# Kernel tuning notes

Hardware: AMD Instinct MI355X
Metric: run time of the kernel (lower is better)

Reference implementation:

```python
import jax, jax.numpy as jnp
import numpy as np

N = 200_000        # primal nodes (mesh faces)
E = 600_000        # directed primal edges (= dual nodes)
F = 128            # feature dim
NUM_KEEP = 300_000 # num_primal_edges_to_keep
ITERS = 40         # label-propagation iterations (>= ~2*log2(N), safely converged)


def setup_inputs() -> dict:
    key = jax.random.key(0)
    k1, k2, k3, k4 = jax.random.split(key, 4)
    primal_x = jax.random.normal(k1, (N, F), dtype=jnp.float32)
    dual_x = jax.random.normal(k2, (E, F), dtype=jnp.float32)
    att = jax.random.uniform(k3, (E,), dtype=jnp.float32)  # attention coeffs in (0,1)
    primal_edge_index = jax.random.randint(k4, (2, E), 0, N, dtype=jnp.int32)
    return {"primal_x": primal_x, "dual_x": dual_x, "att": att,
            "primal_edge_index": primal_edge_index}


def _pool(primal_x, dual_x, att, primal_edge_index):
    src, dst = primal_edge_index[0], primal_edge_index[1]
    num_pool = E - NUM_KEEP

    # --- Top-K edge selection by decreasing attention coefficient ---
    order = jnp.argsort(-att)
    pool_mask = jnp.zeros((E,), jnp.bool_).at[order[:num_pool]].set(True)

    # --- Union-find / connected components of pooled edges via
    #     min-label propagation with pointer jumping (vectorized union-find) ---
    u = src
    v = jnp.where(pool_mask, dst, src)  # masked edges become self-edges (no-ops)

    def body(_, l):
        l = l.at[u].min(l[v]).at[v].min(l[u])  # edge relaxations (scatter-min)
        l = l[l]                                # pointer jumping
        l = l[l]
        return l

    labels = jax.lax.fori_loop(0, ITERS, body, jnp.arange(N, dtype=jnp.int32))

    # --- Compact component labels into contiguous new-primal-node ids ---
    _, cluster = jnp.unique(labels, size=N, fill_value=N, return_inverse=True)
    cluster = cluster.astype(jnp.int32)

    # --- Aggregate primal node features per cluster ('mean') ---
    counts = jax.ops.segment_sum(jnp.ones((N,), primal_x.dtype), cluster,
                                 num_segments=N)
    new_primal_x = jax.ops.segment_sum(primal_x, cluster, num_segments=N)
    new_primal_x = new_primal_x / jnp.maximum(counts, 1.0)[:, None]

    # --- Rebuild primal edges; edges internal to a cluster are pooled away ---
    cu, cv = cluster[src], cluster[dst]
    valid = cu != cv
    new_primal_edge_index = jnp.stack([jnp.where(valid, cu, -1),
                                       jnp.where(valid, cv, -1)])

    # --- Dual nodes: one per (unordered) surviving new primal edge
    #     ('single' dual nodes); merge & mean-aggregate dual features of old
    #     dual nodes mapping to the same new dual node ---
    a = jnp.minimum(cu, cv)
    b = jnp.maximum(cu, cv)
    pairs = jnp.stack([jnp.where(valid, a, N), jnp.where(valid, b, N)], axis=1)
    _, dual_cluster = jnp.unique(pairs, axis=0, size=E, fill_value=N,
                                 return_inverse=True)
    dual_cluster = dual_cluster.reshape(E).astype(jnp.int32)
    vm = valid.astype(dual_x.dtype)
    dcounts = jax.ops.segment_sum(vm, dual_cluster, num_segments=E)
    new_dual_x = jax.ops.segment_sum(dual_x * vm[:, None], dual_cluster,
                                     num_segments=E)
    new_dual_x = new_dual_x / jnp.maximum(dcounts, 1.0)[:, None]

    return new_primal_x, new_dual_x, new_primal_edge_index, cluster


def reference(primal_x, dual_x, att, primal_edge_index):
    return _pool(primal_x, dual_x, att, primal_edge_index)
```

## Files before the change

### kernel.cpp

```cpp
#include <hip/hip_runtime.h>
#include <stdint.h>


#define N_NODES 200000
#define N_EDGES 600000
#define FDIM 128
#define NUM_POOL 300000u

#define SC_NEEDEQ 3
#define SC_TIECNT 4
#define SC_C 5
#define SC_W 6
#define SC_U 7
#define SC_VCNT 8
#define SC_WL0 16
#define TIECAP 4096
#define WLCAP 300800
#define HB 256
#define NSB 98
#define NSHAD 4
#define NSHAD2 16
#define CMAX 16384
#define SROWS 64
#define SGB 782
#define CS2B 128

__device__ __forceinline__ uint32_t f2ou(float f){
  uint32_t b = __float_as_uint(f);
  return (b & 0x80000000u) ? ~b : (b | 0x80000000u);
}

static __device__ __forceinline__ void sel_level(const uint32_t* hist, uint32_t& target,
                                                 uint32_t& pfx, uint32_t* sm, uint32_t* res){
  int t = threadIdx.x;
  uint32_t cnt = hist[t];
  sm[t] = cnt; __syncthreads();
  for(int off = 1; off < 256; off <<= 1){
    uint32_t y = (t + off < 256) ? sm[t + off] : 0u;
    __syncthreads(); sm[t] += y; __syncthreads();
  }
  uint32_t suffix = sm[t];
  uint32_t above  = suffix - cnt;
  if(above < target && target <= suffix){ res[0] = (uint32_t)t; res[1] = target - above; }
  __syncthreads();
  pfx = (pfx << 8) | res[0];
  target = res[1];
  __syncthreads();
}

static __device__ __forceinline__ uint32_t blk_excl(uint32_t v, uint32_t* sm, uint32_t& total){
  int t = threadIdx.x;
  sm[t] = v; __syncthreads();
  for(int off = 1; off < 256; off <<= 1){
    uint32_t y = (t >= off) ? sm[t - off] : 0u;
    __syncthreads(); sm[t] += y; __syncthreads();
  }
  total = sm[255];
  uint32_t incl = sm[t];
  __syncthreads();
  return incl - v;
}

__global__ __launch_bounds__(256) void k_zero(uint4* w4, uint32_t n4){
  uint32_t gid = blockIdx.x*256 + threadIdx.x;
  uint4 z = make_uint4(0u,0u,0u,0u);
  for(uint32_t j = gid; j < n4; j += gridDim.x*256) w4[j] = z;
}

template<int LEVEL>
__global__ __launch_bounds__(256) void k_hist8(const float* att, uint32_t* hists, int* L){
  __shared__ uint32_t h[256];
  __shared__ uint32_t sm[256];
  __shared__ uint32_t res[2];
  h[threadIdx.x] = 0;
  if(LEVEL == 1){
    for(int i = blockIdx.x*256 + threadIdx.x; i < N_NODES; i += HB*256) L[i] = i;
  }
  __syncthreads();
  uint32_t pfx = 0, target = NUM_POOL;
  #pragma unroll
  for(int l = 0; l < LEVEL-1; ++l) sel_level(hists + 256*l, target, pfx, sm, res);
  constexpr int SH1 = (LEVEL > 1) ? 8*(5-LEVEL) : 0;
  constexpr int SH2 = 8*(4-LEVEL);
  for(int e = blockIdx.x*256 + threadIdx.x; e < N_EDGES; e += HB*256){
    uint32_t u = f2ou(att[e]);
    bool ok = (LEVEL == 1) || ((u >> SH1) == pfx);
    if(ok) atomicAdd(&h[(u >> SH2) & 0xFFu], 1u);
  }
  __syncthreads();
  uint32_t c = h[threadIdx.x];
  if(c) atomicAdd(&hists[256*(LEVEL-1) + threadIdx.x], c);
}

__global__ __launch_bounds__(256) void k_seed(const float* att, const int* src, const int* dst,
                       const uint32_t* hists, uint32_t* sc, uint32_t* tieIdx, int* L, uint2* wl,
                       uint32_t* counts, uint32_t* counts2){
  __shared__ uint32_t sm[256];
  __shared__ uint32_t res[2];
  __shared__ uint32_t basesh;
  {
    uint32_t gid = blockIdx.x*256 + threadIdx.x;
    uint32_t gs = gridDim.x*256;
    const uint32_t TOTZ = N_NODES + CMAX*NSHAD2;
    for(uint32_t j = gid; j < TOTZ; j += gs){
      if(j < N_NODES) counts[j] = 0u; else counts2[j - N_NODES] = 0u;
    }
  }
  uint32_t pfx = 0, target = NUM_POOL;
  #pragma unroll
  for(int l = 0; l < 3; ++l) sel_level(hists + 256*l, target, pfx, sm, res);
  if(blockIdx.x == 0 && threadIdx.x == 0) sc[SC_NEEDEQ] = target;
  uint32_t T = pfx;
  int e = blockIdx.x*256 + threadIdx.x;
  bool app = false; int u = 0, v = 0;
  if(e < N_EDGES){
    uint32_t ub = f2ou(att[e]) >> 8;
    if(ub > T){
      u = src[e]; v = dst[e];
      if(u != v){
        int m = u < v ? u : v, hi = u ^ v ^ m;
        atomicMin(&L[hi], m);
        app = true;
      }
    } else if(ub == T){
      uint32_t p = atomicAdd(&sc[SC_TIECNT], 1u);
      if(p < TIECAP) tieIdx[p] = (uint32_t)e;
    }
  }
  uint32_t tot;
  uint32_t off = blk_excl(app ? 1u : 0u, sm, tot);
  if(threadIdx.x == 0 && tot) basesh = atomicAdd(&sc[SC_WL0], tot);
  __syncthreads();
  if(app) wl[basesh + off] = make_uint2((uint32_t)(u < v ? u : v), (uint32_t)(u > v ? u : v));
}

__global__ __launch_bounds__(256) void k_relax(const uint2* wl_in, uint2* wl_out, int* L,
                       uint32_t* sc, int inSlot, int outSlot,
                       const uint32_t* tieIdx, const float* att,
                       const int* src, const int* dst, int doTies){
  __shared__ uint32_t sm[256];
  __shared__ uint32_t basesh;
  uint32_t n = sc[inSlot];
  for(uint32_t base = blockIdx.x*256u; base < n; base += gridDim.x*256u){
    uint32_t idx = base + threadIdx.x;
    bool active = idx < n;
    int lu = 0, lv = 0;
    if(active){
      uint2 ed = wl_in[idx];
      lu = L[ed.x]; lu = L[lu]; lu = L[lu]; lu = L[lu];
      lv = L[ed.y]; lv = L[lv]; lv = L[lv]; lv = L[lv];
      active = (lu != lv);
      if(active){
        int m = lu < lv ? lu : lv, hi = lu ^ lv ^ m;
        atomicMin(&L[hi], m);
      }
    }
    uint32_t tot;
    uint32_t off = blk_excl(active ? 1u : 0u, sm, tot);
    if(threadIdx.x == 0 && tot) basesh = atomicAdd(&sc[outSlot], tot);
    __syncthreads();
    if(active) wl_out[basesh + off] = make_uint2((uint32_t)(lu < lv ? lu : lv),
                                                 (uint32_t)(lu > lv ? lu : lv));
    __syncthreads();
  }
  if(doTies && blockIdx.x == 0){
    uint32_t m = sc[SC_TIECNT]; if(m > TIECAP) m = TIECAP;
    uint32_t need = sc[SC_NEEDEQ];
    for(uint32_t i0 = 0; i0 < m; i0 += 256){
      uint32_t i = i0 + threadIdx.x;
      bool app = false; int u = 0, v = 0;
      if(i < m){
        uint32_t mine = tieIdx[i];
        uint32_t ki = f2ou(att[mine]);
        uint32_t r = 0;
        for(uint32_t j = 0; j < m; j++){
          uint32_t oj = tieIdx[j];
          uint32_t kj = f2ou(att[oj]);
          r += (kj > ki || (kj == ki && oj < mine)) ? 1u : 0u;
        }
        if(r < need){
          u = src[mine]; v = dst[mine];
          if(u != v){ int mm = u < v ? u : v, hi = u ^ v ^ mm; atomicMin(&L[hi], mm); app = true; }
        }
      }
      uint32_t tot;
      uint32_t off = blk_excl(app ? 1u : 0u, sm, tot);
      if(threadIdx.x == 0 && tot) basesh = atomicAdd(&sc[outSlot], tot);
      __syncthreads();
      if(app) wl_out[basesh + off] = make_uint2((uint32_t)(u < v ? u : v),
                                                (uint32_t)(u > v ? u : v));
      __syncthreads();
    }
  }
  if(n != 0){
    int i = blockIdx.x*256 + threadIdx.x;
    if(i < N_NODES){
      int v = L[i]; v = L[v]; v = L[v]; v = L[v];
      if(v < i) atomicMin(&L[i], v);
    }
  }
}
__global__ __launch_bounds__(256) void k_flatten_reduce(int* L, uint32_t* bsums){
  uint32_t base = blockIdx.x*2048u + threadIdx.x*8u;
  uint32_t s = 0;
  #pragma unroll
  for(int k = 0; k < 8; k++){
    uint32_t i = base + k;
    if(i < N_NODES){
      int p = L[i]; int q = L[p];
      while(q != p){ p = q; q = L[p]; }
      L[i] = p;
      s += (p == (int)i) ? 1u : 0u;
    }
  }
  __shared__ uint32_t sm[256];
  sm[threadIdx.x] = s; __syncthreads();
  for(int off = 128; off > 0; off >>= 1){
    if((int)threadIdx.x < off) sm[threadIdx.x] += sm[threadIdx.x + off];
    __syncthreads();
  }
  if(threadIdx.x == 0) bsums[blockIdx.x] = sm[0];
}

template<int MODE>
__device__ __forceinline__ uint32_t scan_n(const uint32_t* sc){
  if(MODE == 1) return sc[SC_W];
  if(MODE == 3) return sc[SC_C]*NSHAD2;
  return N_NODES;
}
template<int MODE>
__global__ __launch_bounds__(256) void k_scan_reduce(const uint32_t* in, uint32_t* bsums,
                       const uint32_t* sc, float* dsum, uint32_t* dcnt){
  uint32_t n = scan_n<MODE>(sc);
  if(MODE == 1){
    uint32_t vc = sc[SC_VCNT];
    size_t gid = (size_t)blockIdx.x*256 + threadIdx.x, gs = (size_t)gridDim.x*256;
    float4* d4 = (float4*)dsum;
    float4 z = make_float4(0.f,0.f,0.f,0.f);
    for(size_t j = gid; j < (size_t)vc*(FDIM/4); j += gs) d4[j] = z;
    for(size_t j = gid; j < vc; j += gs) dcnt[j] = 0u;
  }
  uint32_t base = blockIdx.x*2048u + threadIdx.x*8u;
  uint32_t s = 0;
  #pragma unroll
  for(int k = 0; k < 8; k++){
    uint32_t idx = base + k;
    if(idx < n){ uint32_t v = in[idx]; if(MODE == 1) v = __popc(v); s += v; }
  }
  __shared__ uint32_t sm[256];
  sm[threadIdx.x] = s; __syncthreads();
  for(int off = 128; off > 0; off >>= 1){
    if((int)threadIdx.x < off) sm[threadIdx.x] += sm[threadIdx.x + off];
    __syncthreads();
  }
  if(threadIdx.x == 0) bsums[blockIdx.x] = sm[0];
}
template<int MODE>
__global__ __launch_bounds__(256) void k_scan_apply(const uint32_t* in, const int* L,
                       const uint32_t* bsums, int nb, uint32_t* out, uint32_t* sc){
  __shared__ uint32_t bs[4096];
  __shared__ uint32_t sm[256];
  int t = threadIdx.x;
  uint32_t n = scan_n<MODE>(sc);
  uint32_t loc[16]; uint32_t ls = 0;
  #pragma unroll
  for(int k = 0; k < 16; k++){ int idx = t*16 + k; uint32_t v = (idx < nb) ? bsums[idx] : 0u; loc[k] = v; ls += v; }
  sm[t] = ls; __syncthreads();
  for(int off = 1; off < 256; off <<= 1){
    uint32_t y = (t >= off) ? sm[t - off] : 0u;
    __syncthreads(); sm[t] += y; __syncthreads();
  }
  uint32_t total = sm[255];
  uint32_t run = sm[t] - ls;
  #pragma unroll
  for(int k = 0; k < 16; k++){ bs[t*16 + k] = run; run += loc[k]; }
  __syncthreads();
  uint32_t blockbase = bs[blockIdx.x];
  __syncthreads();
  uint32_t base = blockIdx.x*2048u + t*8u;
  uint32_t xs[8]; uint32_t ts2 = 0;
  #pragma unroll
  for(int k = 0; k < 8; k++){
    uint32_t idx = base + k; uint32_t v = 0;
    if(idx < n){
      if(MODE == 2) v = (L[idx] == (int)idx) ? 1u : 0u;
      else { v = in[idx]; if(MODE == 1) v = __popc(v); }
    }
    xs[k] = v; ts2 += v;
  }
  sm[t] = ts2; __syncthreads();
  for(int off = 1; off < 256; off <<= 1){
    uint32_t y = (t >= off) ? sm[t - off] : 0u;
    __syncthreads(); sm[t] += y; __syncthreads();
  }
  uint32_t run2 = blockbase + sm[t] - ts2;
  #pragma unroll
  for(int k = 0; k < 8; k++){ uint32_t idx = base + k; if(idx < n) out[idx] = run2; run2 += xs[k]; }
  if(blockIdx.x == 0 && t == 0){
    if(MODE == 2){ sc[SC_C] = total; uint64_t cc = (uint64_t)total*(uint64_t)total; sc[SC_W] = (uint32_t)((cc + 31ull) >> 5); }
    if(MODE == 1){ sc[SC_U] = total; }
  }
}

__global__ __launch_bounds__(256) void k_cluster_counts(const int* L, const uint32_t* rank_,
                       int* cluster_i, float* outC, uint32_t* counts, uint32_t* counts2,
                       float* psumS, uint32_t* bitmap, const uint32_t* sc){
  uint32_t C = sc[SC_C], W = sc[SC_W];
  uint32_t gid = blockIdx.x*256 + threadIdx.x, gs = gridDim.x*256;
  float4* p4 = (float4*)psumS;
  float4 z = make_float4(0.f,0.f,0.f,0.f);
  for(size_t j = gid; j < (size_t)NSHAD*C*(FDIM/4); j += gs) p4[j] = z;
  for(uint32_t j = gid; j < W; j += gs) bitmap[j] = 0u;
  int i = (int)gid;
  int lane = threadIdx.x & 63;
  int sh = (int)((gid >> 6) & (NSHAD2-1));
  int c = -1;
  if(i < N_NODES){
    c = (int)rank_[L[i]];
    cluster_i[i] = c;
    outC[i] = (float)c;
  }
  unsigned long long remaining = __ballot(i < N_NODES);
  while(remaining){
    int leader = __ffsll(remaining) - 1;
    int lc = __shfl(c, leader);
    unsigned long long grp = __ballot(c == lc) & remaining;
    if(lane == leader){
      uint32_t cnt = (uint32_t)__popcll(grp);
      atomicAdd(&counts[lc], cnt);
      atomicAdd(&counts2[lc*NSHAD2 + sh], cnt);
    }
    remaining &= ~grp;
  }
}
__global__ void k_scatter(const int* cluster_i, uint32_t* cursor2, uint32_t* order){
  uint32_t gid = blockIdx.x*256 + threadIdx.x;
  int i = (int)gid;
  int lane = threadIdx.x & 63;
  int sh = (int)((gid >> 6) & (NSHAD2-1));
  int c = (i < N_NODES) ? cluster_i[i] : -1;
  unsigned long long remaining = __ballot(i < N_NODES);
  while(remaining){
    int leader = __ffsll(remaining) - 1;
    int lc = __shfl(c, leader);
    unsigned long long grp = __ballot(c == lc) & remaining;
    int b = 0;
    if(lane == leader) b = (int)atomicAdd(&cursor2[lc*NSHAD2 + sh], (uint32_t)__popcll(grp));
    b = __shfl(b, leader);
    if((grp >> lane) & 1ull){
      uint32_t sub = (uint32_t)__popcll(grp & ((1ull << lane) - 1ull));
      order[(uint32_t)b + sub] = (uint32_t)i;
    }
    remaining &= ~grp;
  }
}

__global__ __launch_bounds__(256) void k_seg_edges(const float* px, const uint32_t* order,
        const int* cluster_i, float* psumS, const int* src, const int* dst, uint32_t* sc,
        float* outE, uint32_t* kc, uint32_t* bitmap){
  if(blockIdx.x < SGB){
    int wave = (int)((blockIdx.x*256u + threadIdx.x) >> 6);
    int lane = threadIdx.x & 63;
    int start = wave * SROWS;
    if(start >= N_NODES) return;
    int cnt = N_NODES - start; if(cnt > SROWS) cnt = SROWS;
    size_t shadBase = (size_t)(wave & (NSHAD-1)) * (size_t)sc[SC_C] * FDIM;
    uint32_t ord0 = 0; int c0 = -1;
    if(lane < cnt){ ord0 = order[start + lane]; c0 = cluster_i[ord0]; }
    float ax = 0.f, ay = 0.f; int cur = -1;
    for(int r = 0; r < cnt; r++){
      uint32_t i = (uint32_t)__shfl((int)ord0, r);
      int c = __shfl(c0, r);
      if(c != cur){
        if(cur >= 0){
          atomicAdd(&psumS[shadBase + (size_t)cur*FDIM + 2*lane], ax);
          atomicAdd(&psumS[shadBase + (size_t)cur*FDIM + 2*lane + 1], ay);
        }
        cur = c; ax = 0.f; ay = 0.f;
      }
      float2 v = ((const float2*)(px + (size_t)i*FDIM))[lane];
      ax += v.x; ay += v.y;
    }
    if(cur >= 0){
      atomicAdd(&psumS[shadBase + (size_t)cur*FDIM + 2*lane], ax);
      atomicAdd(&psumS[shadBase + (size_t)cur*FDIM + 2*lane + 1], ay);
    }
  } else {
    __shared__ uint32_t wsum[4];
    int e = (blockIdx.x - SGB)*256 + threadIdx.x;
    int lane = threadIdx.x & 63;
    int wv = threadIdx.x >> 6;
    bool val = false;
    if(e < N_EDGES){
      int cu = cluster_i[src[e]];
      int cv = cluster_i[dst[e]];
      val = (cu != cv);
      outE[e] = val ? (float)cu : -1.0f;
      outE[N_EDGES + e] = val ? (float)cv : -1.0f;
      if(val){
        int a = cu < cv ? cu : cv, b = cu < cv ? cv : cu;
        uint32_t C = sc[SC_C];
        uint32_t key = (uint32_t)a * C + (uint32_t)b;
        kc[e] = key;
        atomicOr(&bitmap[key >> 5], 1u << (key & 31u));
      } else {
        kc[e] = 0xFFFFFFFFu;
      }
    }
    unsigned long long grp = __ballot(val);
    if(lane == 0) wsum[wv] = (uint32_t)__popcll(grp);
    __syncthreads();
    if(threadIdx.x == 0){
      uint32_t s = wsum[0] + wsum[1] + wsum[2] + wsum[3];
      if(s) atomicAdd(&sc[SC_VCNT], s);
    }
  }
}

__global__ __launch_bounds__(256) void k_dualacc(const float* dx, const uint32_t* kc,
                          const uint32_t* bitmap, const uint32_t* wpref,
                          float* dsum, uint32_t* dcnt){
  int wave = (int)((blockIdx.x*256u + threadIdx.x) >> 6);
  int lane = threadIdx.x & 63;
  int base = wave * 64;
  if(base >= N_EDGES) return;
  int e = base + lane;
  uint32_t key = (e < N_EDGES) ? kc[e] : 0xFFFFFFFFu;
  bool val = (key != 0xFFFFFFFFu);
  uint32_t r = 0;
  if(val){
    uint32_t wi = key >> 5, bi = key & 31u;
    r = wpref[wi] + __popc(bitmap[wi] & ((1u << bi) - 1u));
  }
  unsigned long long m = __ballot(val);
  while(m){
    int b = __ffsll(m) - 1;
    m &= m - 1;
    uint32_t ee = (uint32_t)(base + b);
    uint32_t rr = (uint32_t)__shfl((int)r, b);
    float2 v = ((const float2*)(dx + (size_t)ee*FDIM))[lane];
    atomicAdd(&dsum[(size_t)rr*FDIM + 2*lane], v.x);
    atomicAdd(&dsum[(size_t)rr*FDIM + 2*lane + 1], v.y);
    if(lane == 0) atomicAdd(&dcnt[rr], 1u);
  }
}
__global__ __launch_bounds__(256) void k_finalize(const float4* psumS, const uint32_t* counts,
        const float4* dsum, const uint32_t* dcnt, const uint32_t* sc, float4* out4){
  uint32_t C = sc[SC_C], U = sc[SC_U];
  size_t cs = (size_t)C * (FDIM/4);
  size_t gid = (size_t)blockIdx.x*256 + threadIdx.x;
  size_t gs = (size_t)gridDim.x*256;
  const size_t NP4 = (size_t)N_NODES*(FDIM/4);
  const size_t TOT4 = (size_t)(N_NODES + N_EDGES)*(FDIM/4);
  for(size_t j = gid; j < TOT4; j += gs){
    float4 v = make_float4(0.f,0.f,0.f,0.f);
    if(j < NP4){
      uint32_t r = (uint32_t)(j >> 5);
      if(r < C){
        v = psumS[j];
        #pragma unroll
        for(int s = 1; s < NSHAD; s++){
          float4 t = psumS[(size_t)s*cs + j];
          v.x += t.x; v.y += t.y; v.z += t.z; v.w += t.w;
        }
        float fc = (float)counts[r];
        v.x /= fc; v.y /= fc; v.z /= fc; v.w /= fc;
      }
    } else {
      size_t dj = j - NP4;
      uint32_t r = (uint32_t)(dj >> 5);
      if(r < U){
        v = dsum[dj];
        float fc = (float)dcnt[r];
        v.x /= fc; v.y /= fc; v.z /= fc; v.w /= fc;
      }
    }
    out4[j] = v;
  }
}

extern "C" void kernel_launch(void* const* d_in, const int* in_sizes, int n_in,
                              void* d_out, int out_size, void* d_ws, size_t ws_size,
                              hipStream_t stream){
  (void)in_sizes; (void)n_in; (void)out_size;
  const float* primal_x = (const float*)d_in[0];
  const float* dual_x   = (const float*)d_in[1];
  const float* att      = (const float*)d_in[2];
  const int*   pei      = (const int*)d_in[3];
  const int* src = pei;
  const int* dst = pei + N_EDGES;

  float* out  = (float*)d_out;
  float* outE = out + (size_t)(N_NODES + N_EDGES)*FDIM;
  float* outC = outE + (size_t)2*N_EDGES;

  uint32_t* w = (uint32_t*)d_ws;
  size_t words_avail = ws_size / 4;
  const size_t PSUMW = (size_t)NSHAD*CMAX*FDIM;
  const size_t CNT2W = (size_t)CMAX*NSHAD2;
  const size_t FIXED = 64 + 1024 + (size_t)N_NODES + CNT2W
                     + TIECAP + 4*(size_t)N_NODES + CNT2W + 4*(size_t)WLCAP
                     + (size_t)N_EDGES + (size_t)N_EDGES
                     + 4096
                     + PSUMW + (size_t)N_EDGES*FDIM;
  size_t wcap = (words_avail > FIXED) ? (words_avail - FIXED)/2 : 4;
  if(wcap > 8388608) wcap = 8388608;
  wcap &= ~(size_t)3;

  size_t o = 0;
  uint32_t* sc      = w;               o += 64;
  uint32_t* hists   = w + o;           o += 1024;
  size_t zero_words = o;
  uint32_t* counts  = w + o;           o += N_NODES;
  uint32_t* counts2 = w + o;           o += CNT2W;
  uint32_t* tieIdx  = w + o;           o += TIECAP;
  int* labels       = (int*)(w + o);   o += N_NODES;
  uint32_t* rank_   = w + o;           o += N_NODES;
  int* cluster_i    = (int*)(w + o);   o += N_NODES;
  uint32_t* order   = w + o;           o += N_NODES;
  uint32_t* cursor2 = w + o;           o += CNT2W;
  uint2* wl0        = (uint2*)(w + o); o += 2*(size_t)WLCAP;
  uint2* wl1        = (uint2*)(w + o); o += 2*(size_t)WLCAP;
  uint32_t* kc      = w + o;           o += N_EDGES;
  uint32_t* dcnt    = w + o;           o += N_EDGES;
  uint32_t* bsums   = w + o;           o += 4096;
  float* psumS      = (float*)(w + o); o += PSUMW;
  float* dsum       = (float*)(w + o); o += (size_t)N_EDGES*FDIM;
  uint32_t* bitmap  = w + o;           o += wcap;
  uint32_t* wpref   = w + o;           o += wcap;

  const int EB  = (N_EDGES + 255)/256;
  const int NB  = (N_NODES + 255)/256;
  const int WSB = (int)((wcap + 2047)/2048);

  k_zero<<<2,256,0,stream>>>((uint4*)w, (uint32_t)(zero_words/4));
  k_hist8<1><<<HB,256,0,stream>>>(att, hists, labels);
  k_hist8<2><<<HB,256,0,stream>>>(att, hists, labels);
  k_hist8<3><<<HB,256,0,stream>>>(att, hists, labels);
  k_seed<<<EB,256,0,stream>>>(att, src, dst, hists, sc, tieIdx, labels, wl0, counts, counts2);
  for(int r = 1; r <= 8; ++r){
    uint2* win  = (r & 1) ? wl0 : wl1;
    uint2* wout = (r & 1) ? wl1 : wl0;
    k_relax<<<1024,256,0,stream>>>(win, wout, labels, sc, SC_WL0 + r - 1, SC_WL0 + r,
                                   tieIdx, att, src, dst, (r == 1) ? 1 : 0);
  }
  k_flatten_reduce<<<NSB,256,0,stream>>>(labels, bsums);
  k_scan_apply<2><<<NSB,256,0,stream>>>(counts, labels, bsums, NSB, rank_, sc);
  k_cluster_counts<<<NB,256,0,stream>>>(labels, rank_, cluster_i, outC, counts, counts2,
                                        psumS, bitmap, sc);
  k_scan_reduce<3><<<CS2B,256,0,stream>>>(counts2, bsums, sc, dsum, dcnt);
  k_scan_apply<3><<<CS2B,256,0,stream>>>(counts2, labels, bsums, CS2B, cursor2, sc);
  k_scatter<<<NB,256,0,stream>>>(cluster_i, cursor2, order);
  k_seg_edges<<<SGB + EB,256,0,stream>>>(primal_x, order, cluster_i, psumS,
                                         src, dst, sc, outE, kc, bitmap);
  k_scan_reduce<1><<<WSB,256,0,stream>>>(bitmap, bsums, sc, dsum, dcnt);
  k_scan_apply<1><<<WSB,256,0,stream>>>(bitmap, labels, bsums, WSB, wpref, sc);
  k_dualacc<<<EB,256,0,stream>>>(dual_x, kc, bitmap, wpref, dsum, dcnt);
  k_finalize<<<2048,256,0,stream>>>((const float4*)psumS, counts, (const float4*)dsum,
                                    dcnt, sc, (float4*)out);
}
```

Before: 589.8 us.

## Replace counting-sort node grouping with per-wave bitonic sort and segmented accumulation

Drops the shadow-count histogram, its two scan kernels and the scatter kernel that built a cluster-sorted node order. Each wave now sorts its 64 node ids by cluster with an in-register bitonic sort and accumulates feature runs directly into the shadowed partial sums, also adding the cluster counts. The psum zeroing moves into the seed kernel, and the edge work becomes a separate kernel. This removes several launches and passes over memory. In exchange, runs only span 64 consecutive nodes instead of globally sorted order, so more atomics may hit large clusters, and the seed kernel now zeroes the full CMAX-sized psum buffer.

```diff
diff --git a/kernel.cpp b/kernel.cpp
--- a/kernel.cpp
+++ b/kernel.cpp
@@ -19,11 +19,7 @@
 #define HB 256
 #define NSB 98
 #define NSHAD 4
-#define NSHAD2 16
 #define CMAX 16384
-#define SROWS 64
-#define SGB 782
-#define CS2B 128
 
 __device__ __forceinline__ uint32_t f2ou(float f){
   uint32_t b = __float_as_uint(f);
@@ -94,17 +90,18 @@
 
 __global__ __launch_bounds__(256) void k_seed(const float* att, const int* src, const int* dst,
                        const uint32_t* hists, uint32_t* sc, uint32_t* tieIdx, int* L, uint2* wl,
-                       uint32_t* counts, uint32_t* counts2){
+                       uint32_t* counts, float* psumS){
   __shared__ uint32_t sm[256];
   __shared__ uint32_t res[2];
   __shared__ uint32_t basesh;
   {
     uint32_t gid = blockIdx.x*256 + threadIdx.x;
     uint32_t gs = gridDim.x*256;
-    const uint32_t TOTZ = N_NODES + CMAX*NSHAD2;
-    for(uint32_t j = gid; j < TOTZ; j += gs){
-      if(j < N_NODES) counts[j] = 0u; else counts2[j - N_NODES] = 0u;
-    }
+    for(uint32_t j = gid; j < N_NODES; j += gs) counts[j] = 0u;
+    uint4* p4 = (uint4*)psumS;
+    uint4 z = make_uint4(0u,0u,0u,0u);
+    const uint32_t P4 = (uint32_t)NSHAD*CMAX*(FDIM/4);
+    for(uint32_t j = gid; j < P4; j += gs) p4[j] = z;
   }
   uint32_t pfx = 0, target = NUM_POOL;
   #pragma unroll
@@ -225,7 +222,6 @@
 template<int MODE>
 __device__ __forceinline__ uint32_t scan_n(const uint32_t* sc){
   if(MODE == 1) return sc[SC_W];
-  if(MODE == 3) return sc[SC_C]*NSHAD2;
   return N_NODES;
 }
 template<int MODE>
@@ -302,118 +298,87 @@
   }
 }
 
-__global__ __launch_bounds__(256) void k_cluster_counts(const int* L, const uint32_t* rank_,
-                       int* cluster_i, float* outC, uint32_t* counts, uint32_t* counts2,
+__global__ __launch_bounds__(256) void k_cluster_seg(const int* L, const uint32_t* rank_,
+                       const float* px, int* cluster_i, float* outC, uint32_t* counts,
                        float* psumS, uint32_t* bitmap, const uint32_t* sc){
-  uint32_t C = sc[SC_C], W = sc[SC_W];
+  uint32_t W = sc[SC_W];
   uint32_t gid = blockIdx.x*256 + threadIdx.x, gs = gridDim.x*256;
-  float4* p4 = (float4*)psumS;
-  float4 z = make_float4(0.f,0.f,0.f,0.f);
-  for(size_t j = gid; j < (size_t)NSHAD*C*(FDIM/4); j += gs) p4[j] = z;
   for(uint32_t j = gid; j < W; j += gs) bitmap[j] = 0u;
+  int lane = (int)(threadIdx.x & 63);
+  int wave = (int)(gid >> 6);
   int i = (int)gid;
-  int lane = threadIdx.x & 63;
-  int sh = (int)((gid >> 6) & (NSHAD2-1));
-  int c = -1;
-  if(i < N_NODES){
-    c = (int)rank_[L[i]];
+  bool act = i < N_NODES;
+  int key = 0x7FFFFFFF; uint32_t val = 0;
+  if(act){
+    int c = (int)rank_[L[i]];
     cluster_i[i] = c;
     outC[i] = (float)c;
-  }
-  unsigned long long remaining = __ballot(i < N_NODES);
-  while(remaining){
-    int leader = __ffsll(remaining) - 1;
-    int lc = __shfl(c, leader);
-    unsigned long long grp = __ballot(c == lc) & remaining;
-    if(lane == leader){
-      uint32_t cnt = (uint32_t)__popcll(grp);
-      atomicAdd(&counts[lc], cnt);
-      atomicAdd(&counts2[lc*NSHAD2 + sh], cnt);
-    }
-    remaining &= ~grp;
-  }
-}
-__global__ void k_scatter(const int* cluster_i, uint32_t* cursor2, uint32_t* order){
-  uint32_t gid = blockIdx.x*256 + threadIdx.x;
-  int i = (int)gid;
+    key = c; val = (uint32_t)i;
+  }
+  if(__ballot(act) == 0ull) return;
+  #pragma unroll
+  for(int k = 2; k <= 64; k <<= 1){
+    #pragma unroll
+    for(int j = k >> 1; j > 0; j >>= 1){
+      int ok = __shfl_xor(key, j);
+      uint32_t ov = (uint32_t)__shfl_xor((int)val, j);
+      bool up = ((lane & k) == 0);
+      bool keepMin = (((lane & j) == 0) == up);
+      if((key > ok) == keepMin){ key = ok; val = ov; }
+    }
+  }
+  size_t shadBase = (size_t)(wave & (NSHAD-1)) * (size_t)sc[SC_C] * FDIM;
+  float ax = 0.f, ay = 0.f; int cur = -1; uint32_t runLen = 0;
+  for(int r = 0; r < 64; r++){
+    int c = __shfl(key, r);
+    uint32_t ii = (uint32_t)__shfl((int)val, r);
+    if(c != cur){
+      if(cur >= 0){
+        atomicAdd(&psumS[shadBase + (size_t)cur*FDIM + 2*lane], ax);
+        atomicAdd(&psumS[shadBase + (size_t)cur*FDIM + 2*lane + 1], ay);
+        if(lane == 0) atomicAdd(&counts[cur], runLen);
+      }
+      cur = c; ax = 0.f; ay = 0.f; runLen = 0;
+    }
+    float2 v = ((const float2*)(px + (size_t)ii*FDIM))[lane];
+    ax += v.x; ay += v.y; runLen++;
+  }
+  if(cur >= 0){
+    atomicAdd(&psumS[shadBase + (size_t)cur*FDIM + 2*lane], ax);
+    atomicAdd(&psumS[shadBase + (size_t)cur*FDIM + 2*lane + 1], ay);
+    if(lane == 0) atomicAdd(&counts[cur], runLen);
+  }
+}
+
+__global__ __launch_bounds__(256) void k_edges(const int* src, const int* dst,
+        const int* cluster_i, uint32_t* sc, float* outE, uint32_t* kc, uint32_t* bitmap){
+  __shared__ uint32_t wsum[4];
+  int e = blockIdx.x*256 + threadIdx.x;
   int lane = threadIdx.x & 63;
-  int sh = (int)((gid >> 6) & (NSHAD2-1));
-  int c = (i < N_NODES) ? cluster_i[i] : -1;
-  unsigned long long remaining = __ballot(i < N_NODES);
-  while(remaining){
-    int leader = __ffsll(remaining) - 1;
-    int lc = __shfl(c, leader);
-    unsigned long long grp = __ballot(c == lc) & remaining;
-    int b = 0;
-    if(lane == leader) b = (int)atomicAdd(&cursor2[lc*NSHAD2 + sh], (uint32_t)__popcll(grp));
-    b = __shfl(b, leader);
-    if((grp >> lane) & 1ull){
-      uint32_t sub = (uint32_t)__popcll(grp & ((1ull << lane) - 1ull));
-      order[(uint32_t)b + sub] = (uint32_t)i;
-    }
-    remaining &= ~grp;
-  }
-}
-
-__global__ __launch_bounds__(256) void k_seg_edges(const float* px, const uint32_t* order,
-        const int* cluster_i, float* psumS, const int* src, const int* dst, uint32_t* sc,
-        float* outE, uint32_t* kc, uint32_t* bitmap){
-  if(blockIdx.x < SGB){
-    int wave = (int)((blockIdx.x*256u + threadIdx.x) >> 6);
-    int lane = threadIdx.x & 63;
-    int start = wave * SROWS;
-    if(start >= N_NODES) return;
-    int cnt = N_NODES - start; if(cnt > SROWS) cnt = SROWS;
-    size_t shadBase = (size_t)(wave & (NSHAD-1)) * (size_t)sc[SC_C] * FDIM;
-    uint32_t ord0 = 0; int c0 = -1;
-    if(lane < cnt){ ord0 = order[start + lane]; c0 = cluster_i[ord0]; }
-    float ax = 0.f, ay = 0.f; int cur = -1;
-    for(int r = 0; r < cnt; r++){
-      uint32_t i = (uint32_t)__shfl((int)ord0, r);
-      int c = __shfl(c0, r);
-      if(c != cur){
-        if(cur >= 0){
-          atomicAdd(&psumS[shadBase + (size_t)cur*FDIM + 2*lane], ax);
-          atomicAdd(&psumS[shadBase + (size_t)cur*FDIM + 2*lane + 1], ay);
-        }
-        cur = c; ax = 0.f; ay = 0.f;
-      }
-      float2 v = ((const float2*)(px + (size_t)i*FDIM))[lane];
-      ax += v.x; ay += v.y;
-    }
-    if(cur >= 0){
-      atomicAdd(&psumS[shadBase + (size_t)cur*FDIM + 2*lane], ax);
-      atomicAdd(&psumS[shadBase + (size_t)cur*FDIM + 2*lane + 1], ay);
-    }
-  } else {
-    __shared__ uint32_t wsum[4];
-    int e = (blockIdx.x - SGB)*256 + threadIdx.x;
-    int lane = threadIdx.x & 63;
-    int wv = threadIdx.x >> 6;
-    bool val = false;
-    if(e < N_EDGES){
-      int cu = cluster_i[src[e]];
-      int cv = cluster_i[dst[e]];
-      val = (cu != cv);
-      outE[e] = val ? (float)cu : -1.0f;
-      outE[N_EDGES + e] = val ? (float)cv : -1.0f;
-      if(val){
-        int a = cu < cv ? cu : cv, b = cu < cv ? cv : cu;
-        uint32_t C = sc[SC_C];
-        uint32_t key = (uint32_t)a * C + (uint32_t)b;
-        kc[e] = key;
-        atomicOr(&bitmap[key >> 5], 1u << (key & 31u));
-      } else {
-        kc[e] = 0xFFFFFFFFu;
-      }
-    }
-    unsigned long long grp = __ballot(val);
-    if(lane == 0) wsum[wv] = (uint32_t)__popcll(grp);
-    __syncthreads();
-    if(threadIdx.x == 0){
-      uint32_t s = wsum[0] + wsum[1] + wsum[2] + wsum[3];
-      if(s) atomicAdd(&sc[SC_VCNT], s);
-    }
+  int wv = threadIdx.x >> 6;
+  bool val = false;
+  if(e < N_EDGES){
+    int cu = cluster_i[src[e]];
+    int cv = cluster_i[dst[e]];
+    val = (cu != cv);
+    outE[e] = val ? (float)cu : -1.0f;
+    outE[N_EDGES + e] = val ? (float)cv : -1.0f;
+    if(val){
+      int a = cu < cv ? cu : cv, b = cu < cv ? cv : cu;
+      uint32_t C = sc[SC_C];
+      uint32_t key = (uint32_t)a * C + (uint32_t)b;
+      kc[e] = key;
+      atomicOr(&bitmap[key >> 5], 1u << (key & 31u));
+    } else {
+      kc[e] = 0xFFFFFFFFu;
+    }
+  }
+  unsigned long long grp = __ballot(val);
+  if(lane == 0) wsum[wv] = (uint32_t)__popcll(grp);
+  __syncthreads();
+  if(threadIdx.x == 0){
+    uint32_t s = wsum[0] + wsum[1] + wsum[2] + wsum[3];
+    if(s) atomicAdd(&sc[SC_VCNT], s);
   }
 }
 
@@ -497,9 +462,8 @@
   uint32_t* w = (uint32_t*)d_ws;
   size_t words_avail = ws_size / 4;
   const size_t PSUMW = (size_t)NSHAD*CMAX*FDIM;
-  const size_t CNT2W = (size_t)CMAX*NSHAD2;
-  const size_t FIXED = 64 + 1024 + (size_t)N_NODES + CNT2W
-                     + TIECAP + 4*(size_t)N_NODES + CNT2W + 4*(size_t)WLCAP
+  const size_t FIXED = 64 + 1024 + (size_t)N_NODES
+                     + TIECAP + 3*(size_t)N_NODES + 4*(size_t)WLCAP
                      + (size_t)N_EDGES + (size_t)N_EDGES
                      + 4096
                      + PSUMW + (size_t)N_EDGES*FDIM;
@@ -512,13 +476,10 @@
   uint32_t* hists   = w + o;           o += 1024;
   size_t zero_words = o;
   uint32_t* counts  = w + o;           o += N_NODES;
-  uint32_t* counts2 = w + o;           o += CNT2W;
   uint32_t* tieIdx  = w + o;           o += TIECAP;
   int* labels       = (int*)(w + o);   o += N_NODES;
   uint32_t* rank_   = w + o;           o += N_NODES;
   int* cluster_i    = (int*)(w + o);   o += N_NODES;
-  uint32_t* order   = w + o;           o += N_NODES;
-  uint32_t* cursor2 = w + o;           o += CNT2W;
   uint2* wl0        = (uint2*)(w + o); o += 2*(size_t)WLCAP;
   uint2* wl1        = (uint2*)(w + o); o += 2*(size_t)WLCAP;
   uint32_t* kc      = w + o;           o += N_EDGES;
@@ -537,7 +498,7 @@
   k_hist8<1><<<HB,256,0,stream>>>(att, hists, labels);
   k_hist8<2><<<HB,256,0,stream>>>(att, hists, labels);
   k_hist8<3><<<HB,256,0,stream>>>(att, hists, labels);
-  k_seed<<<EB,256,0,stream>>>(att, src, dst, hists, sc, tieIdx, labels, wl0, counts, counts2);
+  k_seed<<<EB,256,0,stream>>>(att, src, dst, hists, sc, tieIdx, labels, wl0, counts, psumS);
   for(int r = 1; r <= 8; ++r){
     uint2* win  = (r & 1) ? wl0 : wl1;
     uint2* wout = (r & 1) ? wl1 : wl0;
@@ -546,13 +507,9 @@
   }
   k_flatten_reduce<<<NSB,256,0,stream>>>(labels, bsums);
   k_scan_apply<2><<<NSB,256,0,stream>>>(counts, labels, bsums, NSB, rank_, sc);
-  k_cluster_counts<<<NB,256,0,stream>>>(labels, rank_, cluster_i, outC, counts, counts2,
-                                        psumS, bitmap, sc);
-  k_scan_reduce<3><<<CS2B,256,0,stream>>>(counts2, bsums, sc, dsum, dcnt);
-  k_scan_apply<3><<<CS2B,256,0,stream>>>(counts2, labels, bsums, CS2B, cursor2, sc);
-  k_scatter<<<NB,256,0,stream>>>(cluster_i, cursor2, order);
-  k_seg_edges<<<SGB + EB,256,0,stream>>>(primal_x, order, cluster_i, psumS,
-                                         src, dst, sc, outE, kc, bitmap);
+  k_cluster_seg<<<NB,256,0,stream>>>(labels, rank_, primal_x, cluster_i, outC,
+                                     counts, psumS, bitmap, sc);
+  k_edges<<<EB,256,0,stream>>>(src, dst, cluster_i, sc, outE, kc, bitmap);
   k_scan_reduce<1><<<WSB,256,0,stream>>>(bitmap, bsums, sc, dsum, dcnt);
   k_scan_apply<1><<<WSB,256,0,stream>>>(bitmap, labels, bsums, WSB, wpref, sc);
   k_dualacc<<<EB,256,0,stream>>>(dual_x, kc, bitmap, wpref, dsum, dcnt);
```

New measurement: 508.7 us. -13.8%, faster.
